# Optimization experiments

Hardware: AMD Instinct MI355X
Metric: run time of the kernel (lower is better)

## Reference

```python
import jax, jax.numpy as jnp
import numpy as np

D_MODEL = 1024
N_HEADS = 16
HEAD_DIM = D_MODEL // N_HEADS
B, T = 4, 2048


def setup_inputs() -> dict:
    key = jax.random.key(0)
    k_x, k_qw, k_qb, k_ow, k_ob = jax.random.split(key, 5)
    x = jax.random.normal(k_x, (B, T, D_MODEL), dtype=jnp.float32)
    # torch nn.Linear weights: [out_features, in_features]
    s = 1.0 / np.sqrt(D_MODEL)
    qkv_w = jax.random.uniform(k_qw, (3 * D_MODEL, D_MODEL), jnp.float32, -s, s)
    qkv_b = jax.random.uniform(k_qb, (3 * D_MODEL,), jnp.float32, -s, s)
    out_w = jax.random.uniform(k_ow, (D_MODEL, D_MODEL), jnp.float32, -s, s)
    out_b = jax.random.uniform(k_ob, (D_MODEL,), jnp.float32, -s, s)
    mask = jnp.tril(jnp.ones((T, T), dtype=jnp.int32))[None, None]  # [1,1,T,T] causal
    return {"x": x, "qkv_w": qkv_w, "qkv_b": qkv_b, "out_w": out_w, "out_b": out_b, "mask": mask}


def reference(x, qkv_w, qkv_b, out_w, out_b, mask):
    Bs, Ts, C = x.shape
    qkv = x @ qkv_w.T + qkv_b  # [B,T,3C]
    q, k, v = jnp.split(qkv, 3, axis=-1)
    # [B,T,C] -> [B,H,T,Dh]
    def heads(t):
        return t.reshape(Bs, Ts, N_HEADS, HEAD_DIM).transpose(0, 2, 1, 3)
    q, k, v = heads(q), heads(k), heads(v)
    scale = 1.0 / np.sqrt(HEAD_DIM).astype(np.float32)
    attn = jnp.einsum('bhqd,bhkd->bhqk', q, k) * scale  # [B,H,T,T]
    attn = jnp.where(mask == 0, jnp.finfo(attn.dtype).min, attn)
    attn = jax.nn.softmax(attn, axis=-1)
    y = jnp.einsum('bhqk,bhkd->bhqd', attn, v)  # [B,H,T,Dh]
    y = y.transpose(0, 2, 1, 3).reshape(Bs, Ts, C)
    return y @ out_w.T + out_b
```

## Files before the change

kernel.cpp:

```cpp
#include <hip/hip_runtime.h>
#include <hip/hip_bf16.h>
#include <stdint.h>

#define BB 4
#define TT 2048
#define CC 1024
#define HH 16
#define DH 64
#define MM (BB*TT)
#define NQKV (3*CC)

typedef __attribute__((ext_vector_type(8))) short bf16x8;
typedef __attribute__((ext_vector_type(4))) float f32x4;

#define GLL16(g, l) __builtin_amdgcn_global_load_lds( \
  (const __attribute__((address_space(1))) unsigned int*)(g), \
  (__attribute__((address_space(3))) unsigned int*)(l), 16, 0, 0)

#define EXP2(x) __builtin_amdgcn_exp2f(x)

#define GSLOT(row, lgrp) \
  ((size_t)(((row) >> 1) * 8 + ((((row) & 1) * 4 + (lgrp)) ^ (((row) >> 1) & 7))) * 16)

__device__ inline unsigned short f2b(float f) {
  __hip_bfloat16 h = __float2bfloat16(f);
  return *reinterpret_cast<unsigned short*>(&h);
}

__global__ __launch_bounds__(256) void cvt3(
    const float* __restrict__ a, int na, unsigned short* __restrict__ da,
    const float* __restrict__ b, int nb, unsigned short* __restrict__ db,
    const float* __restrict__ c, int nc, unsigned short* __restrict__ dc) {
  const int stride = gridDim.x * 256 * 4;
  const int base = (blockIdx.x * 256 + threadIdx.x) * 4;
  for (int i = base; i < na; i += stride) {
    float4 v = *reinterpret_cast<const float4*>(a + i);
    ushort4 o; o.x = f2b(v.x); o.y = f2b(v.y); o.z = f2b(v.z); o.w = f2b(v.w);
    *reinterpret_cast<ushort4*>(da + i) = o;
  }
  for (int i = base; i < nb; i += stride) {
    float4 v = *reinterpret_cast<const float4*>(b + i);
    ushort4 o; o.x = f2b(v.x); o.y = f2b(v.y); o.z = f2b(v.z); o.w = f2b(v.w);
    *reinterpret_cast<ushort4*>(db + i) = o;
  }
  for (int i = base; i < nc; i += stride) {
    float4 v = *reinterpret_cast<const float4*>(c + i);
    ushort4 o; o.x = f2b(v.x); o.y = f2b(v.y); o.z = f2b(v.z); o.w = f2b(v.w);
    *reinterpret_cast<ushort4*>(dc + i) = o;
  }
}

__device__ __attribute__((always_inline)) inline void gemm_stage(
    const unsigned short* __restrict__ A, const unsigned short* __restrict__ Bt,
    int bm0, int bn0, int kt, char* sAb, char* sBb, int tid, int wid) {
#pragma unroll
  for (int j = 0; j < 2; ++j) {
    int c = j * 256 + tid;
    int line = c >> 3;
    int u = (c & 7) ^ (line & 7);
    int row = line * 2 + (u >> 2);
    int ks = u & 3;
    const unsigned short* ga = A  + (size_t)(bm0 + row) * 1024 + kt + ks * 8;
    const unsigned short* gb = Bt + (size_t)(bn0 + row) * 1024 + kt + ks * 8;
    GLL16(ga, sAb + j * 4096 + wid * 1024);
    GLL16(gb, sBb + j * 4096 + wid * 1024);
  }
}

#define GEMM_KLOOP(A, Bt, bm0, bn0)                                           \
  gemm_stage(A, Bt, bm0, bn0, 0,  sA,         sB,         tid, wid);          \
  gemm_stage(A, Bt, bm0, bn0, 32, sA + 8192,  sB + 8192,  tid, wid);          \
  gemm_stage(A, Bt, bm0, bn0, 64, sA + 16384, sB + 16384, tid, wid);          \
  asm volatile("s_waitcnt vmcnt(8)" ::: "memory");                            \
  __builtin_amdgcn_s_barrier();                                               \
  int cur = 0;                                                                \
  for (int t = 0; t < 32; ++t) {                                              \
    if (t + 3 < 32) {                                                         \
      const int pb = (cur + 3) & 3;                                           \
      gemm_stage(A, Bt, bm0, bn0, (t + 3) * 32, sA + pb * 8192,               \
                 sB + pb * 8192, tid, wid);                                   \
    }                                                                         \
    const char* cA = sA + cur * 8192;                                         \
    const char* cB = sB + cur * 8192;                                         \
    bf16x8 af[4], bfr[4];                                                     \
    _Pragma("unroll")                                                         \
    for (int mm = 0; mm < 4; ++mm)                                            \
      af[mm] = *reinterpret_cast<const bf16x8*>(cA + GSLOT(wr * 64 + mm * 16 + lrow, lgrp)); \
    _Pragma("unroll")                                                         \
    for (int nn = 0; nn < 4; ++nn)                                            \
      bfr[nn] = *reinterpret_cast<const bf16x8*>(cB + GSLOT(wc * 64 + nn * 16 + lrow, lgrp)); \
    _Pragma("unroll")                                                         \
    for (int mm = 0; mm < 4; ++mm)                                            \
      _Pragma("unroll")                                                       \
      for (int nn = 0; nn < 4; ++nn)                                          \
        acc[mm][nn] = __builtin_amdgcn_mfma_f32_16x16x32_bf16(af[mm], bfr[nn], acc[mm][nn], 0, 0, 0); \
    if (t < 29)       { asm volatile("s_waitcnt vmcnt(8)" ::: "memory"); }    \
    else if (t == 29) { asm volatile("s_waitcnt vmcnt(4)" ::: "memory"); }    \
    else              { asm volatile("s_waitcnt vmcnt(0)" ::: "memory"); }    \
    __builtin_amdgcn_s_barrier();                                             \
    cur = (cur + 1) & 3;                                                      \
  }

__global__ __launch_bounds__(256) void gemm_qkv(
    const unsigned short* __restrict__ A, const unsigned short* __restrict__ Bt,
    const float* __restrict__ bias,
    unsigned short* __restrict__ qd, unsigned short* __restrict__ kd,
    unsigned short* __restrict__ vtd) {
  __shared__ alignas(16) char sA[4 * 8192];
  __shared__ alignas(16) char sB[4 * 8192];
  const int tid = threadIdx.x;
  const int lane = tid & 63, wid = tid >> 6;
  const int wr = wid >> 1, wc = wid & 1;
  const int lrow = lane & 15, lgrp = lane >> 4;
  const int bn0 = blockIdx.x * 128, bm0 = blockIdx.y * 128;
  f32x4 acc[4][4] = {};

  GEMM_KLOOP(A, Bt, bm0, bn0)

  const int part = bn0 >> 10;
#pragma unroll
  for (int mm = 0; mm < 4; ++mm)
#pragma unroll
    for (int nn = 0; nn < 4; ++nn) {
      const int col = bn0 + wc * 64 + nn * 16 + lrow;
      const int cc = col & 1023;
      const int h = cc >> 6, dd = cc & 63;
      const float bv = bias[col];
#pragma unroll
      for (int r = 0; r < 4; ++r) {
        const int row = bm0 + wr * 64 + mm * 16 + lgrp * 4 + r;
        const int b = row >> 11, t = row & 2047;
        float v = acc[mm][nn][r] + bv;
        const size_t bh = (size_t)(b * HH + h);
        if (part == 0)      qd[(bh * TT + t) * DH + dd] = f2b(v * 0.18033688011112042f);
        else if (part == 1) kd[(bh * TT + t) * DH + dd] = f2b(v);
        else {
          const int tp = (t & ~63) | ((t & 15) << 2) | ((t >> 4) & 3);
          vtd[(bh * DH + dd) * TT + tp] = f2b(v);
        }
      }
    }
}

__device__ __attribute__((always_inline)) inline void stage_chunk(
    const unsigned short* kb, const unsigned short* vb, int kv0,
    char* sK, char* sV, int tid, int wid) {
  const int row = tid >> 3;
  const int col = (tid & 7) * 16;
  const int scol = col ^ ((row & 7) << 4);
  GLL16((const char*)kb + (size_t)(kv0 + row) * 128 + scol, sK + wid * 1024);
  GLL16((const char*)vb + (size_t)row * (TT * 2) + (size_t)kv0 * 2 + scol, sV + wid * 1024);
}

__device__ __attribute__((always_inline)) inline void tile_step(
    const bf16x8& qf0, const bf16x8& qf1, f32x4 (&o)[4], float (&lp)[4],
    const char* cK, const char* cV, char* sP, int kv0, int r0, bool diag,
    int lrow, int lgrp) {
  f32x4 s[4];
  __builtin_amdgcn_s_setprio(1);
#pragma unroll
  for (int f = 0; f < 4; ++f) {
    const int key = f * 16 + lrow;
    const char* kr = cK + key * 128;
    const int sw = (key & 7) << 4;
    bf16x8 kf0 = *(const bf16x8*)(kr + ((lgrp * 16) ^ sw));
    bf16x8 kf1 = *(const bf16x8*)(kr + ((64 + lgrp * 16) ^ sw));
    f32x4 z = {};
    z = __builtin_amdgcn_mfma_f32_16x16x32_bf16(qf0, kf0, z, 0, 0, 0);
    s[f] = __builtin_amdgcn_mfma_f32_16x16x32_bf16(qf1, kf1, z, 0, 0, 0);
  }
  __builtin_amdgcn_s_setprio(0);
#pragma unroll
  for (int r = 0; r < 4; ++r) {
    const int qrow = r0 + lgrp * 4 + r;
    float v0 = s[0][r], v1 = s[1][r], v2 = s[2][r], v3 = s[3][r];
    if (diag) {
      v0 = (kv0 +      lrow <= qrow) ? v0 : -1e30f;
      v1 = (kv0 + 16 + lrow <= qrow) ? v1 : -1e30f;
      v2 = (kv0 + 32 + lrow <= qrow) ? v2 : -1e30f;
      v3 = (kv0 + 48 + lrow <= qrow) ? v3 : -1e30f;
    }
    const float p0 = EXP2(v0), p1 = EXP2(v1);
    const float p2 = EXP2(v2), p3 = EXP2(v3);
    lp[r] += (p0 + p1) + (p2 + p3);
    const int rw = lgrp * 4 + r;
    const int rb = rw * 128;
    const int sw = (rw & 7) << 4;
    ushort4 pk;
    pk.x = f2b(p0); pk.y = f2b(p1); pk.z = f2b(p2); pk.w = f2b(p3);
    *(ushort4*)(sP + rb + ((lrow * 8) ^ sw)) = pk;
  }
  const int prb = lrow * 128;
  const int psw = (lrow & 7) << 4;
  bf16x8 pf0 = *(const bf16x8*)(sP + prb + ((lgrp * 16) ^ psw));
  bf16x8 pf1 = *(const bf16x8*)(sP + prb + ((64 + lgrp * 16) ^ psw));
  __builtin_amdgcn_s_setprio(1);
#pragma unroll
  for (int nn = 0; nn < 4; ++nn) {
    const int d = nn * 16 + lrow;
    const char* vr = cV + d * 128;
    const int vsw = (d & 7) << 4;
    bf16x8 vf0 = *(const bf16x8*)(vr + ((lgrp * 16) ^ vsw));
    bf16x8 vf1 = *(const bf16x8*)(vr + ((64 + lgrp * 16) ^ vsw));
    o[nn] = __builtin_amdgcn_mfma_f32_16x16x32_bf16(pf0, vf0, o[nn], 0, 0, 0);
    o[nn] = __builtin_amdgcn_mfma_f32_16x16x32_bf16(pf1, vf1, o[nn], 0, 0, 0);
  }
  __builtin_amdgcn_s_setprio(0);
}

__device__ __attribute__((always_inline)) inline void store_frag(
    unsigned short* __restrict__ outb, const f32x4 (&o)[4], const float (&lp)[4],
    int b, int h, int r0, int lrow, int lgrp) {
#pragma unroll
  for (int r = 0; r < 4; ++r) {
    float t = lp[r];
#pragma unroll
    for (int off = 8; off; off >>= 1) t += __shfl_xor(t, off, 64);
    const float inv = 1.f / t;
    const int qrow = r0 + lgrp * 4 + r;
#pragma unroll
    for (int nn = 0; nn < 4; ++nn)
      outb[((size_t)(b * TT + qrow)) * CC + h * DH + nn * 16 + lrow] = f2b(o[nn][r] * inv);
  }
}

__global__ __launch_bounds__(512, 2) void attn_k(
    const unsigned short* __restrict__ q, const unsigned short* __restrict__ k,
    const unsigned short* __restrict__ vt, unsigned short* __restrict__ outb) {
  const int tid = threadIdx.x;
  const int lane = tid & 63, wid = tid >> 6;
  const int lrow = lane & 15, lgrp = lane >> 4;
  const int bid = blockIdx.x;
  const int bh = bid >> 3;
  const int pr = bid & 7;
  const int b = bh >> 4, h = bh & 15;
  const int qt_lo = pr, qt_hi = 15 - pr;
  const int n_ch = 2 * (qt_hi + 1);
  const int lo_last = 2 * qt_lo + 1;

  __shared__ alignas(16) char smem[65536];
  char* sK = smem;
  char* sV = smem + 24576;
  char* sP = smem + 49152 + wid * 2048;

  const unsigned short* qb = q + (size_t)bh * TT * DH;
  const unsigned short* kb = k + (size_t)bh * TT * DH;
  const unsigned short* vb = vt + (size_t)bh * DH * TT;

  const int r0_lo = qt_lo * 128 + wid * 16;
  const int r0_hi = qt_hi * 128 + wid * 16;

  bf16x8 qlo0 = *(const bf16x8*)&qb[(size_t)(r0_lo + lrow) * DH + lgrp * 8];
  bf16x8 qlo1 = *(const bf16x8*)&qb[(size_t)(r0_lo + lrow) * DH + 32 + lgrp * 8];
  bf16x8 qhi0 = *(const bf16x8*)&qb[(size_t)(r0_hi + lrow) * DH + lgrp * 8];
  bf16x8 qhi1 = *(const bf16x8*)&qb[(size_t)(r0_hi + lrow) * DH + 32 + lgrp * 8];

  f32x4 olo[4] = {}, ohi[4] = {};
  float llo[4] = {0.f, 0.f, 0.f, 0.f}, lhi[4] = {0.f, 0.f, 0.f, 0.f};

  stage_chunk(kb, vb, 0,  sK,        sV,        tid, wid);
  stage_chunk(kb, vb, 64, sK + 8192, sV + 8192, tid, wid);
  asm volatile("s_waitcnt vmcnt(2)" ::: "memory");
  __builtin_amdgcn_s_barrier();

  int cur = 0;
  for (int ci = 0; ci < n_ch; ++ci) {
    const bool pre = (ci + 2 < n_ch);
    if (pre) {
      const int pb = cur == 0 ? 2 : cur - 1;
      stage_chunk(kb, vb, (ci + 2) * 64, sK + pb * 8192, sV + pb * 8192, tid, wid);
    }
    const char* cK = sK + cur * 8192;
    const char* cV = sV + cur * 8192;
    const int kv0 = ci * 64;
    if (ci <= lo_last)
      tile_step(qlo0, qlo1, olo, llo, cK, cV, sP, kv0, r0_lo, kv0 + 63 > r0_lo, lrow, lgrp);
    tile_step(qhi0, qhi1, ohi, lhi, cK, cV, sP, kv0, r0_hi, kv0 + 63 > r0_hi, lrow, lgrp);
    if (pre) { asm volatile("s_waitcnt vmcnt(2)" ::: "memory"); }
    else     { asm volatile("s_waitcnt vmcnt(0)" ::: "memory"); }
    __builtin_amdgcn_s_barrier();
    cur = cur == 2 ? 0 : cur + 1;
  }

  store_frag(outb, olo, llo, b, h, r0_lo, lrow, lgrp);
  store_frag(outb, ohi, lhi, b, h, r0_hi, lrow, lgrp);
}

__global__ __launch_bounds__(256) void gemm_proj(
    const unsigned short* __restrict__ A, const unsigned short* __restrict__ Bt,
    const float* __restrict__ bias, float* __restrict__ out) {
  __shared__ alignas(16) char sA[4 * 8192];
  __shared__ alignas(16) char sB[4 * 8192];
  const int tid = threadIdx.x;
  const int lane = tid & 63, wid = tid >> 6;
  const int wr = wid >> 1, wc = wid & 1;
  const int lrow = lane & 15, lgrp = lane >> 4;
  const int bn0 = blockIdx.x * 128, bm0 = blockIdx.y * 128;
  f32x4 acc[4][4] = {};

  GEMM_KLOOP(A, Bt, bm0, bn0)

#pragma unroll
  for (int mm = 0; mm < 4; ++mm)
#pragma unroll
    for (int nn = 0; nn < 4; ++nn) {
      const int col = bn0 + wc * 64 + nn * 16 + lrow;
      const float bv = bias[col];
#pragma unroll
      for (int r = 0; r < 4; ++r) {
        const int row = bm0 + wr * 64 + mm * 16 + lgrp * 4 + r;
        out[(size_t)row * 1024 + col] = acc[mm][nn][r] + bv;
      }
    }
}

extern "C" void kernel_launch(void* const* d_in, const int* in_sizes, int n_in,
                              void* d_out, int out_size, void* d_ws, size_t ws_size,
                              hipStream_t stream) {
  const float* x     = (const float*)d_in[0];
  const float* qkv_w = (const float*)d_in[1];
  const float* qkv_b = (const float*)d_in[2];
  const float* out_w = (const float*)d_in[3];
  const float* out_b = (const float*)d_in[4];
  float* out = (float*)d_out;
  char* ws = (char*)d_ws;

  unsigned short* xb  = (unsigned short*)(ws);
  unsigned short* att = (unsigned short*)(ws);
  unsigned short* wq  = (unsigned short*)(ws + 16777216);
  unsigned short* wo  = (unsigned short*)(ws + 23068672);
  unsigned short* qd  = (unsigned short*)(ws + 25165824);
  unsigned short* kd  = (unsigned short*)(ws + 41943040);
  unsigned short* vtd = (unsigned short*)(ws + 58720256);

  cvt3<<<2048, 256, 0, stream>>>(x, MM * CC, xb,
                                 qkv_w, NQKV * CC, wq,
                                 out_w, CC * CC, wo);

  gemm_qkv<<<dim3(NQKV / 128, MM / 128), 256, 0, stream>>>(xb, wq, qkv_b, qd, kd, vtd);
  attn_k<<<BB * HH * 8, 512, 0, stream>>>(qd, kd, vtd, att);
  gemm_proj<<<dim3(CC / 128, MM / 128), 256, 0, stream>>>(att, wo, out_b, out);
}
```

Measured before the change: 226.0 us.

## Replace multi-stage LDS pipeline in GEMM k-loop with single-buffer synchronous loads

The QKV and output-projection GEMMs drop their 4-deep shared-memory ring buffer and hand-tuned vmcnt waits. Each k-step now loads one tile into a single buffer, synchronizes, computes, and synchronizes again. This cuts LDS per block from 64KB to 16KB, which may allow more resident blocks per CU. In exchange it gives up overlap between global loads and MFMA work and adds a second barrier per iteration.

```diff
diff --git a/kernel.cpp b/kernel.cpp
--- a/kernel.cpp
+++ b/kernel.cpp
@@ -68,37 +68,22 @@
 }
 
 #define GEMM_KLOOP(A, Bt, bm0, bn0)                                           \
-  gemm_stage(A, Bt, bm0, bn0, 0,  sA,         sB,         tid, wid);          \
-  gemm_stage(A, Bt, bm0, bn0, 32, sA + 8192,  sB + 8192,  tid, wid);          \
-  gemm_stage(A, Bt, bm0, bn0, 64, sA + 16384, sB + 16384, tid, wid);          \
-  asm volatile("s_waitcnt vmcnt(8)" ::: "memory");                            \
-  __builtin_amdgcn_s_barrier();                                               \
-  int cur = 0;                                                                \
-  for (int t = 0; t < 32; ++t) {                                              \
-    if (t + 3 < 32) {                                                         \
-      const int pb = (cur + 3) & 3;                                           \
-      gemm_stage(A, Bt, bm0, bn0, (t + 3) * 32, sA + pb * 8192,               \
-                 sB + pb * 8192, tid, wid);                                   \
-    }                                                                         \
-    const char* cA = sA + cur * 8192;                                         \
-    const char* cB = sB + cur * 8192;                                         \
+  for (int kt = 0; kt < 1024; kt += 32) {                                     \
+    gemm_stage(A, Bt, bm0, bn0, kt, sA, sB, tid, wid);                        \
+    __syncthreads();                                                          \
     bf16x8 af[4], bfr[4];                                                     \
     _Pragma("unroll")                                                         \
     for (int mm = 0; mm < 4; ++mm)                                            \
-      af[mm] = *reinterpret_cast<const bf16x8*>(cA + GSLOT(wr * 64 + mm * 16 + lrow, lgrp)); \
+      af[mm] = *reinterpret_cast<const bf16x8*>(sA + GSLOT(wr * 64 + mm * 16 + lrow, lgrp)); \
     _Pragma("unroll")                                                         \
     for (int nn = 0; nn < 4; ++nn)                                            \
-      bfr[nn] = *reinterpret_cast<const bf16x8*>(cB + GSLOT(wc * 64 + nn * 16 + lrow, lgrp)); \
+      bfr[nn] = *reinterpret_cast<const bf16x8*>(sB + GSLOT(wc * 64 + nn * 16 + lrow, lgrp)); \
     _Pragma("unroll")                                                         \
     for (int mm = 0; mm < 4; ++mm)                                            \
       _Pragma("unroll")                                                       \
       for (int nn = 0; nn < 4; ++nn)                                          \
         acc[mm][nn] = __builtin_amdgcn_mfma_f32_16x16x32_bf16(af[mm], bfr[nn], acc[mm][nn], 0, 0, 0); \
-    if (t < 29)       { asm volatile("s_waitcnt vmcnt(8)" ::: "memory"); }    \
-    else if (t == 29) { asm volatile("s_waitcnt vmcnt(4)" ::: "memory"); }    \
-    else              { asm volatile("s_waitcnt vmcnt(0)" ::: "memory"); }    \
-    __builtin_amdgcn_s_barrier();                                             \
-    cur = (cur + 1) & 3;                                                      \
+    __syncthreads();                                                          \
   }
 
 __global__ __launch_bounds__(256) void gemm_qkv(
@@ -106,8 +91,8 @@
     const float* __restrict__ bias,
     unsigned short* __restrict__ qd, unsigned short* __restrict__ kd,
     unsigned short* __restrict__ vtd) {
-  __shared__ alignas(16) char sA[4 * 8192];
-  __shared__ alignas(16) char sB[4 * 8192];
+  __shared__ alignas(16) char sA[8192];
+  __shared__ alignas(16) char sB[8192];
   const int tid = threadIdx.x;
   const int lane = tid & 63, wid = tid >> 6;
   const int wr = wid >> 1, wc = wid & 1;
@@ -289,8 +274,8 @@
 __global__ __launch_bounds__(256) void gemm_proj(
     const unsigned short* __restrict__ A, const unsigned short* __restrict__ Bt,
     const float* __restrict__ bias, float* __restrict__ out) {
-  __shared__ alignas(16) char sA[4 * 8192];
-  __shared__ alignas(16) char sB[4 * 8192];
+  __shared__ alignas(16) char sA[8192];
+  __shared__ alignas(16) char sB[8192];
   const int tid = threadIdx.x;
   const int lane = tid & 63, wid = tid >> 6;
   const int wr = wid >> 1, wc = wid & 1;
```

New measurement: 208.4 us (median of 11 runs). 7.8% less time.
